# Kernel tuning notes

Hardware: AMD Instinct MI355X
Metric: run time of the kernel (lower is better)

Reference implementation:

```python
import jax, jax.numpy as jnp
import numpy as np

B, T, D = 4, 2048, 1024
H, KVH = 16, 4          # query heads, kv heads
HD = D // H             # head_dim = 64
R = 32                  # partial rope dims
ROPE_BASE = 10000.0
EPS = 1e-6


def rmsnorm(x, scale):
    # per-head RMSNorm over last dim, computed in fp32 like the torch code
    xf = x.astype(jnp.float32)
    norm = jax.lax.rsqrt(jnp.mean(xf * xf, axis=-1, keepdims=True) + EPS)
    return (xf * norm).astype(x.dtype) * scale


def apply_rope(x, cos, sin):
    # x: (B,T,H,HD); rotate first R dims, pass the rest through
    x_r, x_p = x[..., :R], x[..., R:]
    half = R // 2
    x1, x2 = x_r[..., :half], x_r[..., half:]
    rotated = jnp.concatenate([x1 * cos - x2 * sin, x1 * sin + x2 * cos], axis=-1)
    return jnp.concatenate([rotated, x_p], axis=-1)


def setup_inputs() -> dict:
    key = jax.random.key(0)
    ks = jax.random.split(key, 8)
    x = jax.random.normal(ks[0], (B, T, D), dtype=jnp.float32)
    # RoPE tables exactly as RotaryEmbedding.get_cos_sin
    inv_freq = 1.0 / (ROPE_BASE ** (jnp.arange(0, R, 2, dtype=jnp.float32) / R))
    t = jnp.arange(T, dtype=jnp.float32)
    freqs = jnp.outer(t, inv_freq)                      # (T, R/2)
    cos = jnp.cos(freqs)[None, :, None, :]              # (1,T,1,R/2)
    sin = jnp.sin(freqs)[None, :, None, :]
    s = 1.0 / np.sqrt(D)
    Wq = jax.random.normal(ks[1], (D, D), dtype=jnp.float32) * s
    Wk = jax.random.normal(ks[2], (KVH * HD, D), dtype=jnp.float32) * s
    Wv = jax.random.normal(ks[3], (KVH * HD, D), dtype=jnp.float32) * s
    Wo = jax.random.normal(ks[4], (D, D), dtype=jnp.float32) * s
    q_scale = jnp.ones((HD,), dtype=jnp.float32)
    k_scale = jnp.ones((HD,), dtype=jnp.float32)
    return {"x": x, "cos": cos, "sin": sin, "Wq": Wq, "Wk": Wk, "Wv": Wv,
            "Wo": Wo, "q_scale": q_scale, "k_scale": k_scale}


def reference(x, cos, sin, Wq, Wk, Wv, Wo, q_scale, k_scale):
    b, t, d = x.shape
    q = jnp.einsum('btd,ed->bte', x, Wq).reshape(b, t, H, HD)
    k = jnp.einsum('btd,ed->bte', x, Wk).reshape(b, t, KVH, HD)
    v = jnp.einsum('btd,ed->bte', x, Wv).reshape(b, t, KVH, HD)
    q = apply_rope(rmsnorm(q, q_scale), cos, sin)
    k = apply_rope(rmsnorm(k, k_scale), cos, sin)
    groups = H // KVH
    k = jnp.repeat(k, groups, axis=2)   # (b,t,H,HD), matches repeat_interleave dim=2
    v = jnp.repeat(v, groups, axis=2)
    q = q.transpose(0, 2, 1, 3)         # (b,H,t,HD)
    k = k.transpose(0, 2, 1, 3)
    v = v.transpose(0, 2, 1, 3)
    scores = jnp.einsum('bhqd,bhkd->bhqk', q, k) / np.sqrt(HD)
    causal = jnp.tril(jnp.ones((t, t), dtype=bool))
    scores = jnp.where(causal, scores, -jnp.inf)
    attn = jax.nn.softmax(scores, axis=-1)
    y = jnp.einsum('bhqk,bhkd->bhqd', attn, v)
    y = y.transpose(0, 2, 1, 3).reshape(b, t, d)
    return jnp.einsum('btd,ed->bte', y, Wo)
```

## Files before the change

### kernel.cpp

```cpp
#include <hip/hip_runtime.h>
#include <hip/hip_bf16.h>
#include <stdint.h>

typedef __attribute__((ext_vector_type(8)))  __bf16 bf16x8;
typedef __attribute__((ext_vector_type(4)))  float  f32x4;
typedef __attribute__((ext_vector_type(16))) float  f32x16;
typedef __hip_bfloat16 bf16_t;

#define T_SEQ 2048
#define D_MODEL 1024
#define N_HEADS 16
#define N_KV 4
#define HD 64
#define LDQKV 1536
#define KDIM 1024

__device__ inline void cvt16(const float4* __restrict__ g, int4* __restrict__ s) {
  float4 v0 = g[0], v1 = g[1], v2 = g[2], v3 = g[3];
  union { int4 i[2]; __hip_bfloat162 h[8]; } u;
  u.h[0] = __float22bfloat162_rn(make_float2(v0.x, v0.y));
  u.h[1] = __float22bfloat162_rn(make_float2(v0.z, v0.w));
  u.h[2] = __float22bfloat162_rn(make_float2(v1.x, v1.y));
  u.h[3] = __float22bfloat162_rn(make_float2(v1.z, v1.w));
  u.h[4] = __float22bfloat162_rn(make_float2(v2.x, v2.y));
  u.h[5] = __float22bfloat162_rn(make_float2(v2.z, v2.w));
  u.h[6] = __float22bfloat162_rn(make_float2(v3.x, v3.y));
  u.h[7] = __float22bfloat162_rn(make_float2(v3.z, v3.w));
  s[0] = u.i[0]; s[1] = u.i[1];
}

__device__ inline void storeC(bf16_t* p, float v) { *p = __float2bfloat16(v); }
__device__ inline void storeC(float* p, float v) { *p = v; }

__device__ inline void plswap(unsigned& a, unsigned& b) {
  asm volatile("v_permlane32_swap_b32 %0, %1" : "+v"(a), "+v"(b));
}

__device__ inline float fexp2(float x) {
  float r; asm("v_exp_f32 %0, %1" : "=v"(r) : "v"(x)); return r;
}
__device__ inline unsigned cvtpk(float lo, float hi) {
  unsigned r; asm("v_cvt_pk_bf16_f32 %0, %1, %2" : "=v"(r) : "v"(lo), "v"(hi));
  return r;
}

__device__ inline void gll16(const bf16_t* g, bf16_t* l) {
  __builtin_amdgcn_global_load_lds(
      (const __attribute__((address_space(1))) void*)g,
      (__attribute__((address_space(3))) void*)l, 16, 0, 0);
}

__global__ __launch_bounds__(256) void all_cvt(
    const float* __restrict__ x,
    const float* __restrict__ Wq, const float* __restrict__ Wk,
    const float* __restrict__ Wv, const float* __restrict__ Wo,
    bf16_t* __restrict__ xb, bf16_t* __restrict__ wqkvb,
    bf16_t* __restrict__ wob) {
  const int i = blockIdx.x * 256 + threadIdx.x;
  const float* s; bf16_t* d; int off;
  if (i < 524288)      { s = x;  d = xb;                   off = i; }
  else if (i < 589824) { s = Wq; d = wqkvb;                off = i - 524288; }
  else if (i < 606208) { s = Wk; d = wqkvb + 1024 * 1024;  off = i - 589824; }
  else if (i < 622592) { s = Wv; d = wqkvb + 1280 * 1024;  off = i - 606208; }
  else                 { s = Wo; d = wob;                  off = i - 622592; }
  cvt16((const float4*)s + off * 4, (int4*)d + off * 2);
}

template <int MODE, typename CT>
__global__ __launch_bounds__(256) void gemm_bb(
    const bf16_t* __restrict__ A, const bf16_t* __restrict__ W,
    CT* __restrict__ C, const int ldC,
    const float* __restrict__ cosb, const float* __restrict__ sinb,
    const float* __restrict__ qs, const float* __restrict__ ks,
    bf16_t* __restrict__ v_t)
{
  __shared__ bf16_t As[128 * 32];
  __shared__ bf16_t Bs[128 * 32];
  const int tid = threadIdx.x;
  const int lane = tid & 63;
  const int wv = tid >> 6;
  const int wr = wv >> 1, wc = wv & 1;
  const int m0 = blockIdx.y * 128;
  const int n0 = blockIdx.x * 128;

  const int srow = lane >> 2;
  const int scol = (lane & 3) * 8;
  const bf16_t* gA = A + (size_t)(m0 + 32 * wv + srow) * KDIM + scol;
  const bf16_t* gB = W + (size_t)(n0 + 32 * wv + srow) * KDIM + scol;
  bf16_t* lA = As + wv * 1024;
  bf16_t* lB = Bs + wv * 1024;

  f32x4 acc[4][4];
#pragma unroll
  for (int m = 0; m < 4; ++m)
#pragma unroll
    for (int n = 0; n < 4; ++n)
      acc[m][n] = {0.f, 0.f, 0.f, 0.f};

  const int fr = lane & 15;
  const int fq = lane >> 4;

  for (int k0 = 0; k0 < KDIM; k0 += 32) {
    gll16(gA + k0, lA);
    gll16(gA + 16 * KDIM + k0, lA + 512);
    gll16(gB + k0, lB);
    gll16(gB + 16 * KDIM + k0, lB + 512);
    __syncthreads();
    bf16x8 af[4], bfv[4];
#pragma unroll
    for (int m = 0; m < 4; ++m)
      af[m] = *(const bf16x8*)(&As[(wr * 64 + m * 16 + fr) * 32 + fq * 8]);
#pragma unroll
    for (int n = 0; n < 4; ++n)
      bfv[n] = *(const bf16x8*)(&Bs[(wc * 64 + n * 16 + fr) * 32 + fq * 8]);
#pragma unroll
    for (int m = 0; m < 4; ++m)
#pragma unroll
      for (int n = 0; n < 4; ++n)
        acc[m][n] = __builtin_amdgcn_mfma_f32_16x16x32_bf16(af[m], bfv[n],
                                                            acc[m][n], 0, 0, 0);
    __syncthreads();
  }

  if (MODE == 0 || n0 < 1280) {
    if (MODE == 1) {
      const float* stab = (n0 < 1024) ? qs : ks;
      float sc0 = stab[fr], sc1 = stab[16 + fr], sc2 = stab[32 + fr], sc3 = stab[48 + fr];
#pragma unroll
      for (int m = 0; m < 4; ++m)
#pragma unroll
        for (int r = 0; r < 4; ++r) {
          const int row = m0 + wr * 64 + m * 16 + fq * 4 + r;
          const int t = row & (T_SEQ - 1);
          float ss = acc[m][0][r] * acc[m][0][r] + acc[m][1][r] * acc[m][1][r]
                   + acc[m][2][r] * acc[m][2][r] + acc[m][3][r] * acc[m][3][r];
          ss += __shfl_xor(ss, 1);
          ss += __shfl_xor(ss, 2);
          ss += __shfl_xor(ss, 4);
          ss += __shfl_xor(ss, 8);
          const float nrm = rsqrtf(ss * (1.f / 64.f) + 1e-6f);
          const float v0 = acc[m][0][r] * nrm * sc0;
          const float v1 = acc[m][1][r] * nrm * sc1;
          const float v2 = acc[m][2][r] * nrm * sc2;
          const float v3 = acc[m][3][r] * nrm * sc3;
          const float c = cosb[t * 16 + fr];
          const float s = sinb[t * 16 + fr];
          const float r0 = v0 * c - v1 * s;
          const float r1 = v0 * s + v1 * c;
          bf16_t* p = (bf16_t*)C + (size_t)row * ldC + n0 + wc * 64 + fr;
          p[0]  = __float2bfloat16(r0);
          p[16] = __float2bfloat16(r1);
          p[32] = __float2bfloat16(v2);
          p[48] = __float2bfloat16(v3);
        }
    } else {
#pragma unroll
      for (int m = 0; m < 4; ++m)
#pragma unroll
        for (int n = 0; n < 4; ++n)
#pragma unroll
          for (int r = 0; r < 4; ++r) {
            const int row = wr * 64 + m * 16 + fq * 4 + r;
            const int col = wc * 64 + n * 16 + fr;
            storeC(&C[(size_t)(m0 + row) * ldC + n0 + col], acc[m][n][r]);
          }
    }
  } else {
#pragma unroll
    for (int m = 0; m < 4; ++m) {
      const int row0 = m0 + wr * 64 + m * 16 + fq * 4;
      const int b = row0 >> 11, t0 = row0 & (T_SEQ - 1);
#pragma unroll
      for (int n = 0; n < 4; ++n) {
        const int vcol = n0 - 1280 + wc * 64 + n * 16 + fr;
        const int g = b * 4 + (vcol >> 6);
        const int d = vcol & 63;
        uint2 pk2;
        pk2.x = cvtpk(acc[m][n][0], acc[m][n][1]);
        pk2.y = cvtpk(acc[m][n][2], acc[m][n][3]);
        *(uint2*)(v_t + ((size_t)g * HD + d) * T_SEQ + t0) = pk2;
      }
    }
  }
}

__global__ __launch_bounds__(256) void attn(
    const bf16_t* __restrict__ qkv, const bf16_t* __restrict__ v_t,
    bf16_t* __restrict__ y)
{
  __shared__ int4 lds[2048];
  const int tid  = threadIdx.x;
  const int lane = tid & 63;
  const int wv   = tid >> 6;
  const int ql   = lane & 31;
  const int hi   = lane >> 5;
  const int id   = (int)blockIdx.x;
  const int low3 = id & 7;
  const int rest = id >> 3;
  const int gsel = rest & 1;
  const int hh   = (rest >> 1) & 3;
  const int p    = rest >> 3;
  const int g16  = low3 + 8 * gsel;
  const int b    = g16 >> 2, kvh = g16 & 3;
  const int h    = kvh * 4 + hh;
  const int sA   = 4 * p + wv;
  const float SCALE_LOG2 = 0.125f * 1.44269504089f;

  const int kr = tid >> 3, kslot = tid & 7;
  const int vd = tid >> 2, vslot = tid & 3;
  const bf16_t* gK = qkv + (size_t)(b * T_SEQ + kr) * LDQKV + 1024 + kvh * HD + kslot * 8;
  const bf16_t* gV = v_t + (size_t)((b * N_KV + kvh) * HD + vd) * T_SEQ + vslot * 8;
  const int wKidx = kr * 8 + (kslot ^ (kr & 7));
  const int wVidx = 512 + vd * 4 + (vslot ^ ((vd >> 1) & 3));

  int kridx[4];
#pragma unroll
  for (int c = 0; c < 4; ++c)
    kridx[c] = ql * 8 + ((2 * c + hi) ^ (ql & 7));
  const int vsw = (ql >> 1) & 3;
  const int v0idx = 512 + ql * 4 + (hi ^ vsw);
  const int v1idx = 512 + ql * 4 + ((2 + hi) ^ vsw);
  const int v2idx = 512 + (ql + 32) * 4 + (hi ^ vsw);
  const int v3idx = 512 + (ql + 32) * 4 + ((2 + hi) ^ vsw);

  union ob { unsigned u[4]; bf16x8 v; } onesf;
#pragma unroll
  for (int i = 0; i < 4; ++i) onesf.u[i] = 0x3F803F80u;

  f32x16 zro;
#pragma unroll
  for (int i = 0; i < 16; ++i) zro[i] = 0.f;

  int buf = 0;
#pragma unroll
  for (int pi = 0; pi < 2; ++pi) {
    const int s = pi ? (63 - sA) : sA;
    const int q_glob = s * 32 + ql;
    const int nt = s + 1;
    const int nR = pi ? (32 - 2 * p) : (2 * p + 2);

    const bf16_t* Qrow = qkv + (size_t)(b * T_SEQ + q_glob) * LDQKV + h * HD + hi * 8;
    bf16x8 qfrag[4];
#pragma unroll
    for (int c = 0; c < 4; ++c) {
      bf16x8 raw = *(const bf16x8*)(Qrow + c * 16);
      bf16x8 sc;
#pragma unroll
      for (int j = 0; j < 8; ++j)
        sc[j] = (__bf16)((float)raw[j] * SCALE_LOG2);
      qfrag[c] = sc;
    }

    f32x16 acc0, acc1, accL;
#pragma unroll
    for (int i = 0; i < 16; ++i) { acc0[i] = 0.f; acc1[i] = 0.f; accL[i] = 0.f; }
    float m_run = -1e30f;

    {
      int4 kA = *(const int4*)gK;
      int4 vA = *(const int4*)gV;
      int4 kB = *(const int4*)(gK + (size_t)32 * LDQKV);
      int4 vB = *(const int4*)(gV + 32);
      const int nb = buf * 1024;
      lds[nb + wKidx] = kA;       lds[nb + wVidx] = vA;
      lds[nb + 256 + wKidx] = kB; lds[nb + 256 + wVidx] = vB;
    }
    __syncthreads();

    for (int r = 0; r < nR; ++r) {
      int4 kA, vA, kB, vB;
      const bool more = (r + 1 < nR);
      if (more) {
        const size_t kAdv = (size_t)(r + 1) * 64 * LDQKV;
        const int vAdv = (r + 1) * 64;
        kA = *(const int4*)(gK + kAdv);
        vA = *(const int4*)(gV + vAdv);
        kB = *(const int4*)(gK + kAdv + (size_t)32 * LDQKV);
        vB = *(const int4*)(gV + vAdv + 32);
      }

#pragma unroll
      for (int u = 0; u < 2; ++u) {
        const int t = 2 * r + u;
        if (t < nt) {
          const int k0 = t << 5;
          const bool masked = (t == nt - 1);
          const int base = buf * 1024 + u * 256;

          bf16x8 kf0 = *(const bf16x8*)&lds[base + kridx[0]];
          bf16x8 kf1 = *(const bf16x8*)&lds[base + kridx[1]];
          bf16x8 kf2 = *(const bf16x8*)&lds[base + kridx[2]];
          bf16x8 kf3 = *(const bf16x8*)&lds[base + kridx[3]];

          __builtin_amdgcn_s_setprio(1);
          f32x16 st = __builtin_amdgcn_mfma_f32_32x32x16_bf16(kf0, qfrag[0], zro, 0, 0, 0);
          st = __builtin_amdgcn_mfma_f32_32x32x16_bf16(kf1, qfrag[1], st, 0, 0, 0);
          st = __builtin_amdgcn_mfma_f32_32x32x16_bf16(kf2, qfrag[2], st, 0, 0, 0);
          st = __builtin_amdgcn_mfma_f32_32x32x16_bf16(kf3, qfrag[3], st, 0, 0, 0);
          __builtin_amdgcn_s_setprio(0);

          if (masked) {
#pragma unroll
            for (int rr = 0; rr < 16; ++rr) {
              const int kg = k0 + (rr & 3) + 8 * (rr >> 2) + 4 * hi;
              if (kg > q_glob) st[rr] = -1e30f;
            }
          }
          float m01 = fmaxf(fmaxf(st[0], st[1]), st[2]);
          float m02 = fmaxf(fmaxf(st[3], st[4]), st[5]);
          float m03 = fmaxf(fmaxf(st[6], st[7]), st[8]);
          float m04 = fmaxf(fmaxf(st[9], st[10]), st[11]);
          float m05 = fmaxf(fmaxf(st[12], st[13]), st[14]);
          float m06 = fmaxf(fmaxf(m01, m02), m03);
          float m07 = fmaxf(fmaxf(m04, m05), st[15]);
          const float bmax = fmaxf(m06, m07);
          if (__any(bmax > m_run + 8.f)) {
            const float rmax = fmaxf(bmax, __shfl_xor(bmax, 32));
            const float mnew = fmaxf(m_run, rmax);
            const float corr = fexp2(m_run - mnew);
#pragma unroll
            for (int i = 0; i < 16; ++i) { acc0[i] *= corr; acc1[i] *= corr; }
            accL[0] *= corr;
            m_run = mnew;
          }
          float pp[16];
#pragma unroll
          for (int rr = 0; rr < 16; ++rr) pp[rr] = fexp2(st[rr] - m_run);

          unsigned w[8];
#pragma unroll
          for (int i = 0; i < 8; ++i) w[i] = cvtpk(pp[2 * i], pp[2 * i + 1]);
          plswap(w[0], w[2]); plswap(w[1], w[3]);
          plswap(w[4], w[6]); plswap(w[5], w[7]);
          union fu { unsigned u[4]; bf16x8 v; };
          fu f1, f2;
          f1.u[0] = w[0]; f1.u[1] = w[1]; f1.u[2] = w[2]; f1.u[3] = w[3];
          f2.u[0] = w[4]; f2.u[1] = w[5]; f2.u[2] = w[6]; f2.u[3] = w[7];

          bf16x8 vf0 = *(const bf16x8*)&lds[base + v0idx];
          bf16x8 vf1 = *(const bf16x8*)&lds[base + v1idx];
          bf16x8 vf2 = *(const bf16x8*)&lds[base + v2idx];
          bf16x8 vf3 = *(const bf16x8*)&lds[base + v3idx];

          __builtin_amdgcn_s_setprio(1);
          acc0 = __builtin_amdgcn_mfma_f32_32x32x16_bf16(vf0, f1.v, acc0, 0, 0, 0);
          acc0 = __builtin_amdgcn_mfma_f32_32x32x16_bf16(vf1, f2.v, acc0, 0, 0, 0);
          acc1 = __builtin_amdgcn_mfma_f32_32x32x16_bf16(vf2, f1.v, acc1, 0, 0, 0);
          acc1 = __builtin_amdgcn_mfma_f32_32x32x16_bf16(vf3, f2.v, acc1, 0, 0, 0);
          accL = __builtin_amdgcn_mfma_f32_32x32x16_bf16(onesf.v, f1.v, accL, 0, 0, 0);
          accL = __builtin_amdgcn_mfma_f32_32x32x16_bf16(onesf.v, f2.v, accL, 0, 0, 0);
          __builtin_amdgcn_s_setprio(0);
        }
      }

      if (more) {
        const int nb = (buf ^ 1) * 1024;
        lds[nb + wKidx] = kA;       lds[nb + wVidx] = vA;
        lds[nb + 256 + wKidx] = kB; lds[nb + 256 + wVidx] = vB;
      }
      __syncthreads();
      buf ^= 1;
    }

    const float inv = 1.f / accL[0];
    bf16_t* yrow = y + (size_t)(b * T_SEQ + q_glob) * D_MODEL + h * HD;
#pragma unroll
    for (int gg = 0; gg < 4; ++gg) {
      uint2 o0, o1;
      o0.x = cvtpk(acc0[4 * gg + 0] * inv, acc0[4 * gg + 1] * inv);
      o0.y = cvtpk(acc0[4 * gg + 2] * inv, acc0[4 * gg + 3] * inv);
      o1.x = cvtpk(acc1[4 * gg + 0] * inv, acc1[4 * gg + 1] * inv);
      o1.y = cvtpk(acc1[4 * gg + 2] * inv, acc1[4 * gg + 3] * inv);
      *(uint2*)(yrow + 8 * gg + 4 * hi)      = o0;
      *(uint2*)(yrow + 32 + 8 * gg + 4 * hi) = o1;
    }
  }
}

extern "C" void kernel_launch(void* const* d_in, const int* in_sizes, int n_in,
                              void* d_out, int out_size, void* d_ws,
                              size_t ws_size, hipStream_t stream) {
  const float* x    = (const float*)d_in[0];
  const float* cosb = (const float*)d_in[1];
  const float* sinb = (const float*)d_in[2];
  const float* Wq   = (const float*)d_in[3];
  const float* Wk   = (const float*)d_in[4];
  const float* Wv   = (const float*)d_in[5];
  const float* Wo   = (const float*)d_in[6];
  const float* qs   = (const float*)d_in[7];
  const float* ks   = (const float*)d_in[8];
  float* out = (float*)d_out;

  char* ws = (char*)d_ws;
  bf16_t* qkv   = (bf16_t*)ws;
  bf16_t* v_t   = (bf16_t*)(ws + 25165824);
  bf16_t* y     = (bf16_t*)(ws + 29360128);
  bf16_t* xb    = y;
  bf16_t* wqkvb = (bf16_t*)(ws + 46137344);
  bf16_t* wob   = (bf16_t*)(ws + 49283072);

  all_cvt<<<dim3(2688), 256, 0, stream>>>(x, Wq, Wk, Wv, Wo, xb, wqkvb, wob);

  gemm_bb<1, bf16_t><<<dim3(12, 64), 256, 0, stream>>>(
      xb, wqkvb, qkv, LDQKV, cosb, sinb, qs, ks, v_t);
  attn<<<dim3(512), 256, 0, stream>>>(qkv, v_t, y);
  gemm_bb<0, float><<<dim3(8, 64), 256, 0, stream>>>(
      y, wob, out, D_MODEL, nullptr, nullptr, nullptr, nullptr, nullptr);
}
```

Baseline: 163.3 us.

## Split each key tile across two waves in attention and merge partials via LDS

Doubles the attention block to 512 threads so that each 32-row query strip gets two waves. Each wave processes one of the two 32-key halves of every 64-key tile, keeping its own running max, row sum and output accumulators. At the end the two partial softmax states are merged through shared memory, with the odd wave writing its state and the even wave rescaling, combining and storing the result. The aim is more waves in flight and a shorter serial chain per wave, to hide MFMA and exp latency better. The cost is extra barriers and an LDS round-trip for the merge, and each wave now repeats the Q loads and softmax bookkeeping.

Result: no change. 160.3 us (-1.8%).

```diff
diff --git a/kernel.cpp b/kernel.cpp
--- a/kernel.cpp
+++ b/kernel.cpp
@@ -184,14 +184,16 @@
   }
 }
 
-__global__ __launch_bounds__(256) void attn(
+__global__ __launch_bounds__(512) void attn(
     const bf16_t* __restrict__ qkv, const bf16_t* __restrict__ v_t,
     bf16_t* __restrict__ y)
 {
   __shared__ int4 lds[2048];
   const int tid  = threadIdx.x;
   const int lane = tid & 63;
-  const int wv   = tid >> 6;
+  const int w    = tid >> 6;
+  const int spair= w >> 1;
+  const int h    = w & 1;
   const int ql   = lane & 31;
   const int hi   = lane >> 5;
   const int id   = (int)blockIdx.x;
@@ -202,16 +204,18 @@
   const int p    = rest >> 3;
   const int g16  = low3 + 8 * gsel;
   const int b    = g16 >> 2, kvh = g16 & 3;
-  const int h    = kvh * 4 + hh;
-  const int sA   = 4 * p + wv;
+  const int hd   = kvh * 4 + hh;
+  const int sA   = 4 * p + spair;
   const float SCALE_LOG2 = 0.125f * 1.44269504089f;
 
-  const int kr = tid >> 3, kslot = tid & 7;
-  const int vd = tid >> 2, vslot = tid & 3;
-  const bf16_t* gK = qkv + (size_t)(b * T_SEQ + kr) * LDQKV + 1024 + kvh * HD + kslot * 8;
-  const bf16_t* gV = v_t + (size_t)((b * N_KV + kvh) * HD + vd) * T_SEQ + vslot * 8;
-  const int wKidx = kr * 8 + (kslot ^ (kr & 7));
-  const int wVidx = 512 + vd * 4 + (vslot ^ ((vd >> 1) & 3));
+  const int sid = tid & 255;
+  const int u   = tid >> 8;
+  const int kr = sid >> 3, kslot = sid & 7;
+  const int vd = sid >> 2, vslot = sid & 3;
+  const bf16_t* gK = qkv + (size_t)(b * T_SEQ + kr + u * 32) * LDQKV + 1024 + kvh * HD + kslot * 8;
+  const bf16_t* gV = v_t + (size_t)((b * N_KV + kvh) * HD + vd) * T_SEQ + vslot * 8 + u * 32;
+  const int wKidx = u * 256 + kr * 8 + (kslot ^ (kr & 7));
+  const int wVidx = 512 + u * 256 + vd * 4 + (vslot ^ ((vd >> 1) & 3));
 
   int kridx[4];
 #pragma unroll
@@ -223,14 +227,15 @@
   const int v2idx = 512 + (ql + 32) * 4 + (hi ^ vsw);
   const int v3idx = 512 + (ql + 32) * 4 + ((2 + hi) ^ vsw);
 
-  union ob { unsigned u[4]; bf16x8 v; } onesf;
-#pragma unroll
-  for (int i = 0; i < 4; ++i) onesf.u[i] = 0x3F803F80u;
+  union ob { unsigned uu[4]; bf16x8 v; } onesf;
+#pragma unroll
+  for (int i = 0; i < 4; ++i) onesf.uu[i] = 0x3F803F80u;
 
   f32x16 zro;
 #pragma unroll
   for (int i = 0; i < 16; ++i) zro[i] = 0.f;
 
+  float* lf = (float*)lds;
   int buf = 0;
 #pragma unroll
   for (int pi = 0; pi < 2; ++pi) {
@@ -239,7 +244,7 @@
     const int nt = s + 1;
     const int nR = pi ? (32 - 2 * p) : (2 * p + 2);
 
-    const bf16_t* Qrow = qkv + (size_t)(b * T_SEQ + q_glob) * LDQKV + h * HD + hi * 8;
+    const bf16_t* Qrow = qkv + (size_t)(b * T_SEQ + q_glob) * LDQKV + hd * HD + hi * 8;
     bf16x8 qfrag[4];
 #pragma unroll
     for (int c = 0; c < 4; ++c) {
@@ -259,121 +264,144 @@
     {
       int4 kA = *(const int4*)gK;
       int4 vA = *(const int4*)gV;
-      int4 kB = *(const int4*)(gK + (size_t)32 * LDQKV);
-      int4 vB = *(const int4*)(gV + 32);
       const int nb = buf * 1024;
-      lds[nb + wKidx] = kA;       lds[nb + wVidx] = vA;
-      lds[nb + 256 + wKidx] = kB; lds[nb + 256 + wVidx] = vB;
+      lds[nb + wKidx] = kA;
+      lds[nb + wVidx] = vA;
     }
     __syncthreads();
 
     for (int r = 0; r < nR; ++r) {
-      int4 kA, vA, kB, vB;
+      int4 kA, vA;
       const bool more = (r + 1 < nR);
       if (more) {
-        const size_t kAdv = (size_t)(r + 1) * 64 * LDQKV;
-        const int vAdv = (r + 1) * 64;
-        kA = *(const int4*)(gK + kAdv);
-        vA = *(const int4*)(gV + vAdv);
-        kB = *(const int4*)(gK + kAdv + (size_t)32 * LDQKV);
-        vB = *(const int4*)(gV + vAdv + 32);
+        kA = *(const int4*)(gK + (size_t)(r + 1) * 64 * LDQKV);
+        vA = *(const int4*)(gV + (r + 1) * 64);
       }
 
-#pragma unroll
-      for (int u = 0; u < 2; ++u) {
-        const int t = 2 * r + u;
-        if (t < nt) {
-          const int k0 = t << 5;
-          const bool masked = (t == nt - 1);
-          const int base = buf * 1024 + u * 256;
-
-          bf16x8 kf0 = *(const bf16x8*)&lds[base + kridx[0]];
-          bf16x8 kf1 = *(const bf16x8*)&lds[base + kridx[1]];
-          bf16x8 kf2 = *(const bf16x8*)&lds[base + kridx[2]];
-          bf16x8 kf3 = *(const bf16x8*)&lds[base + kridx[3]];
-
-          __builtin_amdgcn_s_setprio(1);
-          f32x16 st = __builtin_amdgcn_mfma_f32_32x32x16_bf16(kf0, qfrag[0], zro, 0, 0, 0);
-          st = __builtin_amdgcn_mfma_f32_32x32x16_bf16(kf1, qfrag[1], st, 0, 0, 0);
-          st = __builtin_amdgcn_mfma_f32_32x32x16_bf16(kf2, qfrag[2], st, 0, 0, 0);
-          st = __builtin_amdgcn_mfma_f32_32x32x16_bf16(kf3, qfrag[3], st, 0, 0, 0);
-          __builtin_amdgcn_s_setprio(0);
-
-          if (masked) {
-#pragma unroll
-            for (int rr = 0; rr < 16; ++rr) {
-              const int kg = k0 + (rr & 3) + 8 * (rr >> 2) + 4 * hi;
-              if (kg > q_glob) st[rr] = -1e30f;
-            }
+      const int t = 2 * r + h;
+      if (t < nt) {
+        const int k0 = t << 5;
+        const bool masked = (t == nt - 1);
+        const int base = buf * 1024 + h * 256;
+
+        bf16x8 kf0 = *(const bf16x8*)&lds[base + kridx[0]];
+        bf16x8 kf1 = *(const bf16x8*)&lds[base + kridx[1]];
+        bf16x8 kf2 = *(const bf16x8*)&lds[base + kridx[2]];
+        bf16x8 kf3 = *(const bf16x8*)&lds[base + kridx[3]];
+
+        __builtin_amdgcn_s_setprio(1);
+        f32x16 st = __builtin_amdgcn_mfma_f32_32x32x16_bf16(kf0, qfrag[0], zro, 0, 0, 0);
+        st = __builtin_amdgcn_mfma_f32_32x32x16_bf16(kf1, qfrag[1], st, 0, 0, 0);
+        st = __builtin_amdgcn_mfma_f32_32x32x16_bf16(kf2, qfrag[2], st, 0, 0, 0);
+        st = __builtin_amdgcn_mfma_f32_32x32x16_bf16(kf3, qfrag[3], st, 0, 0, 0);
+        __builtin_amdgcn_s_setprio(0);
+
+        if (masked) {
+#pragma unroll
+          for (int rr = 0; rr < 16; ++rr) {
+            const int kg = k0 + (rr & 3) + 8 * (rr >> 2) + 4 * hi;
+            if (kg > q_glob) st[rr] = -1e30f;
           }
-          float m01 = fmaxf(fmaxf(st[0], st[1]), st[2]);
-          float m02 = fmaxf(fmaxf(st[3], st[4]), st[5]);
-          float m03 = fmaxf(fmaxf(st[6], st[7]), st[8]);
-          float m04 = fmaxf(fmaxf(st[9], st[10]), st[11]);
-          float m05 = fmaxf(fmaxf(st[12], st[13]), st[14]);
-          float m06 = fmaxf(fmaxf(m01, m02), m03);
-          float m07 = fmaxf(fmaxf(m04, m05), st[15]);
-          const float bmax = fmaxf(m06, m07);
-          if (__any(bmax > m_run + 8.f)) {
-            const float rmax = fmaxf(bmax, __shfl_xor(bmax, 32));
-            const float mnew = fmaxf(m_run, rmax);
-            const float corr = fexp2(m_run - mnew);
-#pragma unroll
-            for (int i = 0; i < 16; ++i) { acc0[i] *= corr; acc1[i] *= corr; }
-            accL[0] *= corr;
-            m_run = mnew;
-          }
-          float pp[16];
-#pragma unroll
-          for (int rr = 0; rr < 16; ++rr) pp[rr] = fexp2(st[rr] - m_run);
-
-          unsigned w[8];
-#pragma unroll
-          for (int i = 0; i < 8; ++i) w[i] = cvtpk(pp[2 * i], pp[2 * i + 1]);
-          plswap(w[0], w[2]); plswap(w[1], w[3]);
-          plswap(w[4], w[6]); plswap(w[5], w[7]);
-          union fu { unsigned u[4]; bf16x8 v; };
-          fu f1, f2;
-          f1.u[0] = w[0]; f1.u[1] = w[1]; f1.u[2] = w[2]; f1.u[3] = w[3];
-          f2.u[0] = w[4]; f2.u[1] = w[5]; f2.u[2] = w[6]; f2.u[3] = w[7];
-
-          bf16x8 vf0 = *(const bf16x8*)&lds[base + v0idx];
-          bf16x8 vf1 = *(const bf16x8*)&lds[base + v1idx];
-          bf16x8 vf2 = *(const bf16x8*)&lds[base + v2idx];
-          bf16x8 vf3 = *(const bf16x8*)&lds[base + v3idx];
-
-          __builtin_amdgcn_s_setprio(1);
-          acc0 = __builtin_amdgcn_mfma_f32_32x32x16_bf16(vf0, f1.v, acc0, 0, 0, 0);
-          acc0 = __builtin_amdgcn_mfma_f32_32x32x16_bf16(vf1, f2.v, acc0, 0, 0, 0);
-          acc1 = __builtin_amdgcn_mfma_f32_32x32x16_bf16(vf2, f1.v, acc1, 0, 0, 0);
-          acc1 = __builtin_amdgcn_mfma_f32_32x32x16_bf16(vf3, f2.v, acc1, 0, 0, 0);
-          accL = __builtin_amdgcn_mfma_f32_32x32x16_bf16(onesf.v, f1.v, accL, 0, 0, 0);
-          accL = __builtin_amdgcn_mfma_f32_32x32x16_bf16(onesf.v, f2.v, accL, 0, 0, 0);
-          __builtin_amdgcn_s_setprio(0);
         }
+        float m01 = fmaxf(fmaxf(st[0], st[1]), st[2]);
+        float m02 = fmaxf(fmaxf(st[3], st[4]), st[5]);
+        float m03 = fmaxf(fmaxf(st[6], st[7]), st[8]);
+        float m04 = fmaxf(fmaxf(st[9], st[10]), st[11]);
+        float m05 = fmaxf(fmaxf(st[12], st[13]), st[14]);
+        float m06 = fmaxf(fmaxf(m01, m02), m03);
+        float m07 = fmaxf(fmaxf(m04, m05), st[15]);
+        const float bmax = fmaxf(m06, m07);
+        if (__any(bmax > m_run + 8.f)) {
+          const float rmax = fmaxf(bmax, __shfl_xor(bmax, 32));
+          const float mnew = fmaxf(m_run, rmax);
+          const float corr = fexp2(m_run - mnew);
+#pragma unroll
+          for (int i = 0; i < 16; ++i) { acc0[i] *= corr; acc1[i] *= corr; }
+          accL[0] *= corr;
+          m_run = mnew;
+        }
+        float pp[16];
+#pragma unroll
+        for (int rr = 0; rr < 16; ++rr) pp[rr] = fexp2(st[rr] - m_run);
+
+        unsigned wp[8];
+#pragma unroll
+        for (int i = 0; i < 8; ++i) wp[i] = cvtpk(pp[2 * i], pp[2 * i + 1]);
+        plswap(wp[0], wp[2]); plswap(wp[1], wp[3]);
+        plswap(wp[4], wp[6]); plswap(wp[5], wp[7]);
+        union fu { unsigned uu[4]; bf16x8 v; };
+        fu f1, f2;
+        f1.uu[0] = wp[0]; f1.uu[1] = wp[1]; f1.uu[2] = wp[2]; f1.uu[3] = wp[3];
+        f2.uu[0] = wp[4]; f2.uu[1] = wp[5]; f2.uu[2] = wp[6]; f2.uu[3] = wp[7];
+
+        bf16x8 vf0 = *(const bf16x8*)&lds[base + v0idx];
+        bf16x8 vf1 = *(const bf16x8*)&lds[base + v1idx];
+        bf16x8 vf2 = *(const bf16x8*)&lds[base + v2idx];
+        bf16x8 vf3 = *(const bf16x8*)&lds[base + v3idx];
+
+        __builtin_amdgcn_s_setprio(1);
+        acc0 = __builtin_amdgcn_mfma_f32_32x32x16_bf16(vf0, f1.v, acc0, 0, 0, 0);
+        acc0 = __builtin_amdgcn_mfma_f32_32x32x16_bf16(vf1, f2.v, acc0, 0, 0, 0);
+        acc1 = __builtin_amdgcn_mfma_f32_32x32x16_bf16(vf2, f1.v, acc1, 0, 0, 0);
+        acc1 = __builtin_amdgcn_mfma_f32_32x32x16_bf16(vf3, f2.v, acc1, 0, 0, 0);
+        accL = __builtin_amdgcn_mfma_f32_32x32x16_bf16(onesf.v, f1.v, accL, 0, 0, 0);
+        accL = __builtin_amdgcn_mfma_f32_32x32x16_bf16(onesf.v, f2.v, accL, 0, 0, 0);
+        __builtin_amdgcn_s_setprio(0);
       }
 
       if (more) {
         const int nb = (buf ^ 1) * 1024;
-        lds[nb + wKidx] = kA;       lds[nb + wVidx] = vA;
-        lds[nb + 256 + wKidx] = kB; lds[nb + 256 + wVidx] = vB;
+        lds[nb + wKidx] = kA;
+        lds[nb + wVidx] = vA;
       }
       __syncthreads();
       buf ^= 1;
     }
 
-    const float inv = 1.f / accL[0];
-    bf16_t* yrow = y + (size_t)(b * T_SEQ + q_glob) * D_MODEL + h * HD;
-#pragma unroll
-    for (int gg = 0; gg < 4; ++gg) {
-      uint2 o0, o1;
-      o0.x = cvtpk(acc0[4 * gg + 0] * inv, acc0[4 * gg + 1] * inv);
-      o0.y = cvtpk(acc0[4 * gg + 2] * inv, acc0[4 * gg + 3] * inv);
-      o1.x = cvtpk(acc1[4 * gg + 0] * inv, acc1[4 * gg + 1] * inv);
-      o1.y = cvtpk(acc1[4 * gg + 2] * inv, acc1[4 * gg + 3] * inv);
-      *(uint2*)(yrow + 8 * gg + 4 * hi)      = o0;
-      *(uint2*)(yrow + 32 + 8 * gg + 4 * hi) = o1;
-    }
+    float cA = 1.f, cB = 0.f, l_mrg = 0.f;
+    if (h == 1) {
+      const int fb = spair * 1216 + lane * 19;
+#pragma unroll
+      for (int i = 0; i < 16; ++i) lf[fb + i] = acc0[i];
+      lf[fb + 16] = m_run;
+      lf[fb + 17] = accL[0];
+    }
+    __syncthreads();
+    if (h == 0) {
+      const int fb = spair * 1216 + lane * 19;
+      const float mB = lf[fb + 16], lB = lf[fb + 17];
+      const float mM = fmaxf(m_run, mB);
+      cA = fexp2(m_run - mM);
+      cB = fexp2(mB - mM);
+      l_mrg = accL[0] * cA + lB * cB;
+#pragma unroll
+      for (int i = 0; i < 16; ++i) acc0[i] = acc0[i] * cA + lf[fb + i] * cB;
+    }
+    __syncthreads();
+    if (h == 1) {
+      const int fb2 = spair * 1088 + lane * 17;
+#pragma unroll
+      for (int i = 0; i < 16; ++i) lf[fb2 + i] = acc1[i];
+    }
+    __syncthreads();
+    if (h == 0) {
+      const int fb2 = spair * 1088 + lane * 17;
+#pragma unroll
+      for (int i = 0; i < 16; ++i) acc1[i] = acc1[i] * cA + lf[fb2 + i] * cB;
+      const float inv = 1.f / l_mrg;
+      bf16_t* yrow = y + (size_t)(b * T_SEQ + q_glob) * D_MODEL + hd * HD;
+#pragma unroll
+      for (int gg = 0; gg < 4; ++gg) {
+        uint2 o0, o1;
+        o0.x = cvtpk(acc0[4 * gg + 0] * inv, acc0[4 * gg + 1] * inv);
+        o0.y = cvtpk(acc0[4 * gg + 2] * inv, acc0[4 * gg + 3] * inv);
+        o1.x = cvtpk(acc1[4 * gg + 0] * inv, acc1[4 * gg + 1] * inv);
+        o1.y = cvtpk(acc1[4 * gg + 2] * inv, acc1[4 * gg + 3] * inv);
+        *(uint2*)(yrow + 8 * gg + 4 * hi)      = o0;
+        *(uint2*)(yrow + 32 + 8 * gg + 4 * hi) = o1;
+      }
+    }
+    __syncthreads();
   }
 }
 
@@ -403,7 +431,7 @@
 
   gemm_bb<1, bf16_t><<<dim3(12, 64), 256, 0, stream>>>(
       xb, wqkvb, qkv, LDQKV, cosb, sinb, qs, ks, v_t);
-  attn<<<dim3(512), 256, 0, stream>>>(qkv, v_t, y);
+  attn<<<dim3(512), 512, 0, stream>>>(qkv, v_t, y);
   gemm_bb<0, float><<<dim3(8, 64), 256, 0, stream>>>(
       y, wob, out, D_MODEL, nullptr, nullptr, nullptr, nullptr, nullptr);
 }
```
